# Kernel optimization log

Hardware: AMD Instinct MI355X
Metric: run time of the kernel (lower is better)

Reference implementation:

```python
import jax, jax.numpy as jnp
import numpy as np

N_NODES = 100000
N_EDGES = 3200000
DIM = 128
N_LAYERS = 3
NUM_GRAPHS = 128
BN_EPS = 1e-5
GIN_EPS = 0.0  # eps buffer initialized to 0, train_eps=False


def setup_inputs() -> dict:
    key = jax.random.key(0)
    ks = jax.random.split(key, 12)
    s = 1.0 / np.sqrt(DIM)
    inp = {
        "x": jax.random.normal(ks[0], (N_NODES, DIM), jnp.float32),
        "edge_index": jax.random.randint(ks[1], (2, N_EDGES), 0, N_NODES, jnp.int64),
        "batch": jnp.sort(jax.random.randint(ks[2], (N_NODES,), 0, NUM_GRAPHS, jnp.int64)),
        # node encoder Linear(x_dim, emb_dim)
        "W_node": jax.random.uniform(ks[3], (DIM, DIM), jnp.float32, -s, s),
        "b_node": jax.random.uniform(ks[4], (DIM,), jnp.float32, -s, s),
        # per-layer MLP: Linear -> BatchNorm -> ReLU -> Linear, stacked over layers
        "W1": jax.random.uniform(ks[5], (N_LAYERS, DIM, DIM), jnp.float32, -s, s),
        "b1": jax.random.uniform(ks[6], (N_LAYERS, DIM), jnp.float32, -s, s),
        "gamma": jnp.ones((N_LAYERS, DIM), jnp.float32),
        "beta": jnp.zeros((N_LAYERS, DIM), jnp.float32),
        "W2": jax.random.uniform(ks[7], (N_LAYERS, DIM, DIM), jnp.float32, -s, s),
        "b2": jax.random.uniform(ks[8], (N_LAYERS, DIM), jnp.float32, -s, s),
    }
    return inp


def _batchnorm(y, gamma, beta):
    # training-mode batch statistics over the node dimension (biased variance)
    mean = jnp.mean(y, axis=0)
    var = jnp.mean(jnp.square(y - mean), axis=0)
    return (y - mean) * jax.lax.rsqrt(var + BN_EPS) * gamma + beta


def reference(x, edge_index, batch, W_node, b_node, W1, b1, gamma, beta, W2, b2):
    src, dst = edge_index[0], edge_index[1]
    n = x.shape[0]
    h = x @ W_node + b_node  # [N, D]
    for i in range(N_LAYERS):
        # GINConv: scatter-add gathered neighbor features, eps-residual, MLP
        agg = jax.ops.segment_sum(h[src], dst, num_segments=n)  # [N, D]
        out = agg + (1.0 + GIN_EPS) * h
        y = out @ W1[i] + b1[i]
        y = jax.nn.relu(_batchnorm(y, gamma[i], beta[i]))
        y = y @ W2[i] + b2[i]
        h = jax.nn.relu(y)  # outer ReLU in Encoder.forward (dropout_p=0)
    # global_add_pool
    return jax.ops.segment_sum(h, batch, num_segments=NUM_GRAPHS)  # [G, D]
```

## Files before the change

kernel.cpp:

```cpp
#include <hip/hip_runtime.h>

#define N_NODES 100000
#define M_PAD   100096
#define N_EDGES 3200000
#define DIM 128
#define N_LAYERS 3
#define NUM_GRAPHS 128
#define BN_EPS 1e-5f

#define DST_SHIFT 7
#define BUCKET_NODES 128
#define N_BUCKETS ((N_NODES + BUCKET_NODES - 1) / BUCKET_NODES)
#define BUCKET_CAP 4864
#define EDGES_PER_BLOCK 16384
#define BIN_BLOCKS ((N_EDGES + EDGES_PER_BLOCK - 1) / EDGES_PER_BLOCK)
#define N_BANDS 64

typedef unsigned int uint32;
typedef unsigned short u16;
typedef __attribute__((ext_vector_type(8))) short bf16x8;
typedef __attribute__((ext_vector_type(4))) float f32x4;

__device__ __forceinline__ float bf2f(u16 u) {
    union { uint32 i; float f; } c;
    c.i = ((uint32)u) << 16;
    return c.f;
}
__device__ __forceinline__ u16 f2bf(float f) {
    union { float f; uint32 i; } c;
    c.f = f;
    uint32 i = c.i;
    return (u16)((i + 0x7FFFu + ((i >> 16) & 1u)) >> 16);
}
__device__ __forceinline__ float lo_bf(uint32 v) {
    union { uint32 i; float f; } c;
    c.i = v << 16;
    return c.f;
}
__device__ __forceinline__ float hi_bf(uint32 v) {
    union { uint32 i; float f; } c;
    c.i = v & 0xFFFF0000u;
    return c.f;
}
__device__ __forceinline__ uint32 pack_bf2(float a, float b) {
    return ((uint32)f2bf(b) << 16) | (uint32)f2bf(a);
}
__device__ __forceinline__ void unpack_add8(float* acc, uint4 v) {
    acc[0] += lo_bf(v.x); acc[1] += hi_bf(v.x);
    acc[2] += lo_bf(v.y); acc[3] += hi_bf(v.y);
    acc[4] += lo_bf(v.z); acc[5] += hi_bf(v.z);
    acc[6] += lo_bf(v.w); acc[7] += hi_bf(v.w);
}

__global__ __launch_bounds__(256) void zero_misc(int* __restrict__ gcur,
                                                 float* __restrict__ bn_stats,
                                                 float* __restrict__ outp,
                                                 uint32* __restrict__ aggpad32) {
    int i = blockIdx.x * 256 + threadIdx.x;
    if (i < N_BUCKETS) gcur[i] = 0;
    if (i < N_LAYERS * 2 * DIM) bn_stats[i] = 0.f;
    if (i < NUM_GRAPHS * DIM) outp[i] = 0.f;
    if (i < (M_PAD - N_NODES) * DIM / 2) aggpad32[i] = 0;
}

__global__ __launch_bounds__(256) void bin_by_dst(const int* __restrict__ src,
                                                  const int* __restrict__ dst,
                                                  int* __restrict__ gcur,
                                                  uint32* __restrict__ packed) {
    __shared__ int cnt[N_BUCKETS];
    __shared__ int cur[N_BUCKETS];
    int t = threadIdx.x;
    int e0 = blockIdx.x * EDGES_PER_BLOCK;
    for (int i = t; i < N_BUCKETS; i += 256) cnt[i] = 0;
    __syncthreads();

    for (int j = 0; j < EDGES_PER_BLOCK / 256; ++j) {
        int e = e0 + j * 256 + t;
        if (e < N_EDGES) atomicAdd(&cnt[dst[e] >> DST_SHIFT], 1);
    }
    __syncthreads();
    for (int i = t; i < N_BUCKETS; i += 256) {
        int c = cnt[i];
        cur[i] = c ? atomicAdd(&gcur[i], c) : 0;
    }
    __syncthreads();
    for (int j = 0; j < EDGES_PER_BLOCK / 256; ++j) {
        int e = e0 + j * 256 + t;
        if (e < N_EDGES) {
            int d = dst[e];
            int b = d >> DST_SHIFT;
            int pos = atomicAdd(&cur[b], 1);
            if (pos < BUCKET_CAP)
                packed[(size_t)b * BUCKET_CAP + pos] =
                    (uint32)src[e] | ((uint32)(d & (BUCKET_NODES - 1)) << 17);
        }
    }
}

__global__ void scan_buckets(const int* __restrict__ gcur, int* __restrict__ obase,
                             int* __restrict__ row_ptr) {
    __shared__ int s[N_BUCKETS];
    int t = threadIdx.x;
    for (int i = t; i < N_BUCKETS; i += 256) {
        int c = gcur[i];
        s[i] = (c > BUCKET_CAP) ? BUCKET_CAP : c;
    }
    __syncthreads();
    if (t == 0) {
        int run = 0;
        for (int i = 0; i < N_BUCKETS; ++i) {
            int c = s[i];
            s[i] = run;
            run += c;
        }
        row_ptr[N_NODES] = run;
    }
    __syncthreads();
    for (int i = t; i < N_BUCKETS; i += 256) obase[i] = s[i];
}

__global__ __launch_bounds__(256) void build_buckets(const uint32* __restrict__ packed,
                                                     const int* __restrict__ gcur,
                                                     const int* __restrict__ obase_arr,
                                                     int* __restrict__ row_ptr,
                                                     int* __restrict__ col_src) {
    __shared__ uint32 ed[BUCKET_CAP];
    __shared__ uint32 ed2[BUCKET_CAP];
    __shared__ int bandcur[N_BANDS];
    __shared__ int ncnt[BUCKET_NODES];
    __shared__ int ncur[BUCKET_NODES];
    int b = blockIdx.x, t = threadIdx.x;
    int cnt = gcur[b];
    if (cnt > BUCKET_CAP) cnt = BUCKET_CAP;
    int obase = obase_arr[b];
    int n0 = b * BUCKET_NODES;

    if (t < N_BANDS) bandcur[t] = 0;
    if (t < BUCKET_NODES) ncnt[t] = 0;
    __syncthreads();

    const uint32* reg = packed + (size_t)b * BUCKET_CAP;
    for (int i = t; i < cnt; i += 256) {
        uint32 v = reg[i];
        ed[i] = v;
        atomicAdd(&bandcur[(v & 0x1FFFFu) >> 11], 1);
        atomicAdd(&ncnt[v >> 17], 1);
    }
    __syncthreads();

    if (t == 0) {
        int run = 0;
        for (int w = 0; w < N_BANDS; ++w) {
            int c = bandcur[w];
            bandcur[w] = run;
            run += c;
        }
    }
    int myc = (t < BUCKET_NODES) ? ncnt[t] : 0;
    if (t < BUCKET_NODES) ncur[t] = myc;
    __syncthreads();
    for (int off = 1; off < BUCKET_NODES; off <<= 1) {
        int v = 0;
        if (t < BUCKET_NODES && t >= off) v = ncur[t - off];
        __syncthreads();
        if (t < BUCKET_NODES) ncur[t] += v;
        __syncthreads();
    }
    if (t < BUCKET_NODES) {
        int excl = ncur[t] - myc;
        ncur[t] = excl;
        int gn = n0 + t;
        if (gn < N_NODES) row_ptr[gn] = obase + excl;
    }
    __syncthreads();

    for (int i = t; i < cnt; i += 256) {
        uint32 v = ed[i];
        int p = atomicAdd(&bandcur[(v & 0x1FFFFu) >> 11], 1);
        ed2[p] = v;
    }
    __syncthreads();

    for (int i = t; i < cnt; i += 256) {
        uint32 v = ed2[i];
        int slot = atomicAdd(&ncur[v >> 17], 1);
        col_src[obase + slot] = (int)(v & 0x1FFFFu);
    }
}

__global__ void cvt_wt_all(const float* __restrict__ Wn, const float* __restrict__ W1,
                           const float* __restrict__ W2, u16* __restrict__ WT) {
    int m = blockIdx.x >> 7, n = blockIdx.x & 127, k = threadIdx.x;
    const float* src = (m == 0) ? Wn
                     : (m <= 3) ? W1 + (size_t)(m - 1) * DIM * DIM
                                : W2 + (size_t)(m - 4) * DIM * DIM;
    int L = n * 256 + k * 2;
    int Ls = L ^ ((n & 7) << 4);
    *(u16*)((char*)WT + (size_t)m * 32768 + Ls) = f2bf(src[(size_t)k * DIM + n]);
}

__global__ __launch_bounds__(256) void aggregate_bf(const u16* __restrict__ h,
                                                    const int* __restrict__ row_ptr,
                                                    const int* __restrict__ col_src,
                                                    u16* __restrict__ agg) {
    int wv = (blockIdx.x * 256 + threadIdx.x) >> 6;
    int lane = threadIdx.x & 63;
    int q = lane >> 4, c = lane & 15;
    if (wv >= N_NODES) return;
    int beg = row_ptr[wv], end = row_ptr[wv + 1];
    const uint4* h4 = (const uint4*)h;

    float acc[8];
#pragma unroll
    for (int j = 0; j < 8; ++j) acc[j] = 0.f;

    if (q == 0) {
        uint4 v = h4[(size_t)wv * 16 + c];
        unpack_add8(acc, v);
    }
    int e = beg + q;
    for (; e + 12 < end; e += 16) {
        int i0 = col_src[e];
        int i1 = col_src[e + 4];
        int i2 = col_src[e + 8];
        int i3 = col_src[e + 12];
        uint4 v0 = h4[(size_t)i0 * 16 + c];
        uint4 v1 = h4[(size_t)i1 * 16 + c];
        uint4 v2 = h4[(size_t)i2 * 16 + c];
        uint4 v3 = h4[(size_t)i3 * 16 + c];
        unpack_add8(acc, v0);
        unpack_add8(acc, v1);
        unpack_add8(acc, v2);
        unpack_add8(acc, v3);
    }
    for (; e < end; e += 4) {
        uint4 v0 = h4[(size_t)col_src[e] * 16 + c];
        unpack_add8(acc, v0);
    }
#pragma unroll
    for (int j = 0; j < 8; ++j) {
        acc[j] += __shfl_xor(acc[j], 16);
        acc[j] += __shfl_xor(acc[j], 32);
    }
    if (q == 0) {
        uint4 o;
        o.x = pack_bf2(acc[0], acc[1]);
        o.y = pack_bf2(acc[2], acc[3]);
        o.z = pack_bf2(acc[4], acc[5]);
        o.w = pack_bf2(acc[6], acc[7]);
        *(uint4*)&agg[(size_t)wv * DIM + c * 8] = o;
    }
}

template <int MODE>
__global__ __launch_bounds__(256) void gemm_v2(const void* __restrict__ Av,
                                               const u16* __restrict__ WTs,
                                               const float* __restrict__ bias,
                                               u16* __restrict__ outp,
                                               float* __restrict__ bn_sum,
                                               float* __restrict__ bn_sumsq,
                                               const float* __restrict__ gamma,
                                               const float* __restrict__ beta) {
    __shared__ u16 sB[DIM * DIM];
    __shared__ float sc_[DIM];
    __shared__ float sh_[DIM];
    __shared__ float ls[4][DIM];
    __shared__ float lq[4][DIM];

    int t = threadIdx.x;
    {
        const uint4* Wg = (const uint4*)WTs;
        uint4* sB4 = (uint4*)sB;
#pragma unroll
        for (int i = 0; i < 8; ++i) sB4[i * 256 + t] = Wg[i * 256 + t];
    }
    if (MODE == 2 && t < DIM) {
        const float invN = 1.0f / (float)N_NODES;
        float mean = bn_sum[t] * invN;
        float var = fmaxf(bn_sumsq[t] * invN - mean * mean, 0.f);
        float rs = rsqrtf(var + BN_EPS);
        float sc = gamma[t] * rs;
        sc_[t] = sc;
        sh_[t] = beta[t] - mean * sc;
    }
    __syncthreads();

    int wid = t >> 6, lane = t & 63;
    int hw = lane >> 4, c = lane & 15;
    int row0 = blockIdx.x * 128 + wid * 32;

    bf16x8 a[2][4];
#pragma unroll
    for (int rf = 0; rf < 2; ++rf) {
        int row = row0 + rf * 16 + c;
#pragma unroll
        for (int ks = 0; ks < 4; ++ks) {
            int k0 = ks * 32 + hw * 8;
            if (MODE == 0) {
                const float* xf = (const float*)Av;
                float4 v0 = make_float4(0.f, 0.f, 0.f, 0.f), v1 = v0;
                if (row < N_NODES) {
                    v0 = *(const float4*)&xf[(size_t)row * DIM + k0];
                    v1 = *(const float4*)&xf[(size_t)row * DIM + k0 + 4];
                }
                union { bf16x8 v; u16 u[8]; } ua;
                ua.u[0] = f2bf(v0.x); ua.u[1] = f2bf(v0.y);
                ua.u[2] = f2bf(v0.z); ua.u[3] = f2bf(v0.w);
                ua.u[4] = f2bf(v1.x); ua.u[5] = f2bf(v1.y);
                ua.u[6] = f2bf(v1.z); ua.u[7] = f2bf(v1.w);
                a[rf][ks] = ua.v;
            } else {
                const u16* Ab = (const u16*)Av;
                bf16x8 av = *(const bf16x8*)&Ab[(size_t)row * DIM + k0];
                if (MODE == 2) {
                    union { bf16x8 v; u16 u[8]; } ua;
                    ua.v = av;
#pragma unroll
                    for (int j = 0; j < 8; ++j) {
                        float f = bf2f(ua.u[j]);
                        f = fmaxf(fmaf(f, sc_[k0 + j], sh_[k0 + j]), 0.f);
                        ua.u[j] = f2bf(f);
                    }
                    av = ua.v;
                }
                a[rf][ks] = av;
            }
        }
    }

    f32x4 acc[2][8];
#pragma unroll
    for (int rf = 0; rf < 2; ++rf)
#pragma unroll
        for (int nf = 0; nf < 8; ++nf) acc[rf][nf] = (f32x4){0.f, 0.f, 0.f, 0.f};

    int swz = (c & 7) << 4;
#pragma unroll
    for (int ks = 0; ks < 4; ++ks) {
#pragma unroll
        for (int nf = 0; nf < 8; ++nf) {
            int L = (nf * 4096 + c * 256 + ks * 64 + hw * 16) ^ swz;
            bf16x8 b = *(const bf16x8*)((const char*)sB + L);
            acc[0][nf] = __builtin_amdgcn_mfma_f32_16x16x32_bf16(a[0][ks], b, acc[0][nf], 0, 0, 0);
            acc[1][nf] = __builtin_amdgcn_mfma_f32_16x16x32_bf16(a[1][ks], b, acc[1][nf], 0, 0, 0);
        }
    }

    float s_[8], q_[8];
#pragma unroll
    for (int nf = 0; nf < 8; ++nf) { s_[nf] = 0.f; q_[nf] = 0.f; }

#pragma unroll
    for (int rf = 0; rf < 2; ++rf) {
        int rbase = row0 + rf * 16 + hw * 4;
#pragma unroll
        for (int nf = 0; nf < 8; ++nf) {
            float bv = bias[nf * 16 + c];
#pragma unroll
            for (int r = 0; r < 4; ++r) {
                float v = acc[rf][nf][r] + bv;
                if (MODE == 2) v = fmaxf(v, 0.f);
                outp[(size_t)(rbase + r) * DIM + nf * 16 + c] = f2bf(v);
                if (MODE == 1) {
                    float m = (rbase + r < N_NODES) ? v : 0.f;
                    s_[nf] += m;
                    q_[nf] += m * m;
                }
            }
        }
    }

    if (MODE == 1) {
#pragma unroll
        for (int nf = 0; nf < 8; ++nf) {
            s_[nf] += __shfl_xor(s_[nf], 16);
            s_[nf] += __shfl_xor(s_[nf], 32);
            q_[nf] += __shfl_xor(q_[nf], 16);
            q_[nf] += __shfl_xor(q_[nf], 32);
        }
        if (lane < 16) {
#pragma unroll
            for (int nf = 0; nf < 8; ++nf) {
                ls[wid][nf * 16 + c] = s_[nf];
                lq[wid][nf * 16 + c] = q_[nf];
            }
        }
        __syncthreads();
        if (t < DIM) {
            atomicAdd(&bn_sum[t], ls[0][t] + ls[1][t] + ls[2][t] + ls[3][t]);
            atomicAdd(&bn_sumsq[t], lq[0][t] + lq[1][t] + lq[2][t] + lq[3][t]);
        }
    }
}

__global__ __launch_bounds__(256) void pool_bf(const u16* __restrict__ h,
                                               const int* __restrict__ batch,
                                               float* __restrict__ out) {
    int wv = (blockIdx.x * 256 + threadIdx.x) >> 6;
    int lane = threadIdx.x & 63;
    int base = wv * 32;
    if (base >= N_NODES) return;
    int end = base + 32;
    if (end > N_NODES) end = N_NODES;
    const uint32* h32 = (const uint32*)h;
    float ax = 0.f, ay = 0.f;
    int curg = batch[base];
    for (int n = base; n < end; ++n) {
        int g = batch[n];
        if (g != curg) {
            atomicAdd(&out[curg * DIM + lane * 2], ax);
            atomicAdd(&out[curg * DIM + lane * 2 + 1], ay);
            ax = 0.f;
            ay = 0.f;
            curg = g;
        }
        uint32 v = h32[(size_t)n * 64 + lane];
        ax += lo_bf(v);
        ay += hi_bf(v);
    }
    atomicAdd(&out[curg * DIM + lane * 2], ax);
    atomicAdd(&out[curg * DIM + lane * 2 + 1], ay);
}

extern "C" void kernel_launch(void* const* d_in, const int* in_sizes, int n_in,
                              void* d_out, int out_size, void* d_ws, size_t ws_size,
                              hipStream_t stream) {
    const float* x     = (const float*)d_in[0];
    const int*   ei    = (const int*)d_in[1];
    const int*   batch = (const int*)d_in[2];
    const float* Wn    = (const float*)d_in[3];
    const float* bnode = (const float*)d_in[4];
    const float* W1    = (const float*)d_in[5];
    const float* b1    = (const float*)d_in[6];
    const float* gamma = (const float*)d_in[7];
    const float* beta  = (const float*)d_in[8];
    const float* W2    = (const float*)d_in[9];
    const float* b2    = (const float*)d_in[10];
    float* out = (float*)d_out;

    const int* e_src = ei;
    const int* e_dst = ei + N_EDGES;

    const size_t MD = (size_t)M_PAD * DIM;
    u16* h   = (u16*)d_ws;
    u16* agg = h + MD;
    u16* y   = agg + MD;
    u16* WT  = y + MD;
    int* row_ptr = (int*)(WT + 7 * DIM * DIM);
    int* col_src = row_ptr + N_NODES + 1;
    int* gcur    = col_src + N_EDGES;
    int* obase   = gcur + N_BUCKETS;
    float* bn_stats = (float*)(obase + N_BUCKETS);
    uint32* packed = (uint32*)y;

    const int GEMM_BLOCKS = M_PAD / 128;
    const int AGG_BLOCKS = (N_NODES * 64 + 255) / 256;
    const int POOL_BLOCKS = (((N_NODES + 31) / 32) * 64 + 255) / 256;

    zero_misc<<<64, 256, 0, stream>>>(gcur, bn_stats, out,
                                      (uint32*)(agg + (size_t)N_NODES * DIM));
    bin_by_dst<<<BIN_BLOCKS, 256, 0, stream>>>(e_src, e_dst, gcur, packed);
    scan_buckets<<<1, 256, 0, stream>>>(gcur, obase, row_ptr);
    build_buckets<<<N_BUCKETS, 256, 0, stream>>>(packed, gcur, obase, row_ptr, col_src);

    cvt_wt_all<<<7 * DIM, DIM, 0, stream>>>(Wn, W1, W2, WT);

    gemm_v2<0><<<GEMM_BLOCKS, 256, 0, stream>>>(x, WT, bnode, h, nullptr,
                                                nullptr, nullptr, nullptr);

    for (int i = 0; i < N_LAYERS; ++i) {
        float* bn_sum = bn_stats + (size_t)i * 2 * DIM;
        float* bn_sumsq = bn_sum + DIM;
        aggregate_bf<<<AGG_BLOCKS, 256, 0, stream>>>(h, row_ptr, col_src, agg);
        gemm_v2<1><<<GEMM_BLOCKS, 256, 0, stream>>>(
            agg, WT + (size_t)(1 + i) * DIM * DIM, b1 + i * DIM, y, bn_sum,
            bn_sumsq, nullptr, nullptr);
        gemm_v2<2><<<GEMM_BLOCKS, 256, 0, stream>>>(
            y, WT + (size_t)(4 + i) * DIM * DIM, b2 + i * DIM, h, bn_sum,
            bn_sumsq, gamma + i * DIM, beta + i * DIM);
    }

    pool_bf<<<POOL_BLOCKS, 256, 0, stream>>>(h, batch, out);
}
```

Before: 615.0 us.

## Aggregate two nodes per 16-lane group and prefetch GEMM A-tiles before weight staging

```diff
diff --git a/kernel.cpp b/kernel.cpp
--- a/kernel.cpp
+++ b/kernel.cpp
@@ -203,53 +203,66 @@
                                                     const int* __restrict__ row_ptr,
                                                     const int* __restrict__ col_src,
                                                     u16* __restrict__ agg) {
-    int wv = (blockIdx.x * 256 + threadIdx.x) >> 6;
-    int lane = threadIdx.x & 63;
-    int q = lane >> 4, c = lane & 15;
-    if (wv >= N_NODES) return;
-    int beg = row_ptr[wv], end = row_ptr[wv + 1];
+    int t = threadIdx.x;
+    int quad = (blockIdx.x * 256 + t) >> 4;
+    int c = t & 15;
+    int nA = quad * 2;
+    if (nA >= N_NODES) return;
+    int nB = nA + 1;
     const uint4* h4 = (const uint4*)h;
 
-    float acc[8];
-#pragma unroll
-    for (int j = 0; j < 8; ++j) acc[j] = 0.f;
-
-    if (q == 0) {
-        uint4 v = h4[(size_t)wv * 16 + c];
-        unpack_add8(acc, v);
-    }
-    int e = beg + q;
-    for (; e + 12 < end; e += 16) {
-        int i0 = col_src[e];
-        int i1 = col_src[e + 4];
-        int i2 = col_src[e + 8];
-        int i3 = col_src[e + 12];
-        uint4 v0 = h4[(size_t)i0 * 16 + c];
-        uint4 v1 = h4[(size_t)i1 * 16 + c];
-        uint4 v2 = h4[(size_t)i2 * 16 + c];
-        uint4 v3 = h4[(size_t)i3 * 16 + c];
-        unpack_add8(acc, v0);
-        unpack_add8(acc, v1);
-        unpack_add8(acc, v2);
-        unpack_add8(acc, v3);
-    }
-    for (; e < end; e += 4) {
-        uint4 v0 = h4[(size_t)col_src[e] * 16 + c];
-        unpack_add8(acc, v0);
-    }
-#pragma unroll
-    for (int j = 0; j < 8; ++j) {
-        acc[j] += __shfl_xor(acc[j], 16);
-        acc[j] += __shfl_xor(acc[j], 32);
-    }
-    if (q == 0) {
-        uint4 o;
-        o.x = pack_bf2(acc[0], acc[1]);
-        o.y = pack_bf2(acc[2], acc[3]);
-        o.z = pack_bf2(acc[4], acc[5]);
-        o.w = pack_bf2(acc[6], acc[7]);
-        *(uint4*)&agg[(size_t)wv * DIM + c * 8] = o;
-    }
+    int begA = row_ptr[nA], endA = row_ptr[nA + 1];
+    int begB = row_ptr[nB], endB = row_ptr[nB + 1];
+    int lenA = endA - begA, lenB = endB - begB;
+    int m = lenA < lenB ? lenA : lenB;
+
+    float a_[8], b_[8];
+#pragma unroll
+    for (int j = 0; j < 8; ++j) { a_[j] = 0.f; b_[j] = 0.f; }
+
+    {
+        uint4 sA = h4[(size_t)nA * 16 + c];
+        uint4 sB = h4[(size_t)nB * 16 + c];
+        unpack_add8(a_, sA);
+        unpack_add8(b_, sB);
+    }
+
+    int i = 0;
+    for (; i + 2 <= m; i += 2) {
+        int iA0 = col_src[begA + i], iA1 = col_src[begA + i + 1];
+        int iB0 = col_src[begB + i], iB1 = col_src[begB + i + 1];
+        uint4 vA0 = h4[(size_t)iA0 * 16 + c];
+        uint4 vB0 = h4[(size_t)iB0 * 16 + c];
+        uint4 vA1 = h4[(size_t)iA1 * 16 + c];
+        uint4 vB1 = h4[(size_t)iB1 * 16 + c];
+        unpack_add8(a_, vA0);
+        unpack_add8(b_, vB0);
+        unpack_add8(a_, vA1);
+        unpack_add8(b_, vB1);
+    }
+    if (i < m) {
+        uint4 vA = h4[(size_t)col_src[begA + i] * 16 + c];
+        uint4 vB = h4[(size_t)col_src[begB + i] * 16 + c];
+        unpack_add8(a_, vA);
+        unpack_add8(b_, vB);
+        ++i;
+    }
+    for (int e = begA + i; e < endA; ++e) {
+        uint4 v = h4[(size_t)col_src[e] * 16 + c];
+        unpack_add8(a_, v);
+    }
+    for (int e = begB + i; e < endB; ++e) {
+        uint4 v = h4[(size_t)col_src[e] * 16 + c];
+        unpack_add8(b_, v);
+    }
+
+    uint4 oA, oB;
+    oA.x = pack_bf2(a_[0], a_[1]); oA.y = pack_bf2(a_[2], a_[3]);
+    oA.z = pack_bf2(a_[4], a_[5]); oA.w = pack_bf2(a_[6], a_[7]);
+    oB.x = pack_bf2(b_[0], b_[1]); oB.y = pack_bf2(b_[2], b_[3]);
+    oB.z = pack_bf2(b_[4], b_[5]); oB.w = pack_bf2(b_[6], b_[7]);
+    *(uint4*)&agg[(size_t)nA * DIM + c * 8] = oA;
+    *(uint4*)&agg[(size_t)nB * DIM + c * 8] = oB;
 }
 
 template <int MODE>
@@ -268,6 +281,33 @@
     __shared__ float lq[4][DIM];
 
     int t = threadIdx.x;
+    int wid = t >> 6, lane = t & 63;
+    int hw = lane >> 4, c = lane & 15;
+    int row0 = blockIdx.x * 128 + wid * 32;
+
+    bf16x8 a[2][4];
+    float4 af[2][4][2];
+#pragma unroll
+    for (int rf = 0; rf < 2; ++rf) {
+        int row = row0 + rf * 16 + c;
+#pragma unroll
+        for (int ks = 0; ks < 4; ++ks) {
+            int k0 = ks * 32 + hw * 8;
+            if (MODE == 0) {
+                const float* xf = (const float*)Av;
+                af[rf][ks][0] = make_float4(0.f, 0.f, 0.f, 0.f);
+                af[rf][ks][1] = af[rf][ks][0];
+                if (row < N_NODES) {
+                    af[rf][ks][0] = *(const float4*)&xf[(size_t)row * DIM + k0];
+                    af[rf][ks][1] = *(const float4*)&xf[(size_t)row * DIM + k0 + 4];
+                }
+            } else {
+                const u16* Ab = (const u16*)Av;
+                a[rf][ks] = *(const bf16x8*)&Ab[(size_t)row * DIM + k0];
+            }
+        }
+    }
+
     {
         const uint4* Wg = (const uint4*)WTs;
         uint4* sB4 = (uint4*)sB;
@@ -285,45 +325,29 @@
     }
     __syncthreads();
 
-    int wid = t >> 6, lane = t & 63;
-    int hw = lane >> 4, c = lane & 15;
-    int row0 = blockIdx.x * 128 + wid * 32;
-
-    bf16x8 a[2][4];
 #pragma unroll
     for (int rf = 0; rf < 2; ++rf) {
-        int row = row0 + rf * 16 + c;
 #pragma unroll
         for (int ks = 0; ks < 4; ++ks) {
             int k0 = ks * 32 + hw * 8;
             if (MODE == 0) {
-                const float* xf = (const float*)Av;
-                float4 v0 = make_float4(0.f, 0.f, 0.f, 0.f), v1 = v0;
-                if (row < N_NODES) {
-                    v0 = *(const float4*)&xf[(size_t)row * DIM + k0];
-                    v1 = *(const float4*)&xf[(size_t)row * DIM + k0 + 4];
-                }
                 union { bf16x8 v; u16 u[8]; } ua;
+                float4 v0 = af[rf][ks][0], v1 = af[rf][ks][1];
                 ua.u[0] = f2bf(v0.x); ua.u[1] = f2bf(v0.y);
                 ua.u[2] = f2bf(v0.z); ua.u[3] = f2bf(v0.w);
                 ua.u[4] = f2bf(v1.x); ua.u[5] = f2bf(v1.y);
                 ua.u[6] = f2bf(v1.z); ua.u[7] = f2bf(v1.w);
                 a[rf][ks] = ua.v;
-            } else {
-                const u16* Ab = (const u16*)Av;
-                bf16x8 av = *(const bf16x8*)&Ab[(size_t)row * DIM + k0];
-                if (MODE == 2) {
-                    union { bf16x8 v; u16 u[8]; } ua;
-                    ua.v = av;
-#pragma unroll
-                    for (int j = 0; j < 8; ++j) {
-                        float f = bf2f(ua.u[j]);
-                        f = fmaxf(fmaf(f, sc_[k0 + j], sh_[k0 + j]), 0.f);
-                        ua.u[j] = f2bf(f);
-                    }
-                    av = ua.v;
+            } else if (MODE == 2) {
+                union { bf16x8 v; u16 u[8]; } ua;
+                ua.v = a[rf][ks];
+#pragma unroll
+                for (int j = 0; j < 8; ++j) {
+                    float f = bf2f(ua.u[j]);
+                    f = fmaxf(fmaf(f, sc_[k0 + j], sh_[k0 + j]), 0.f);
+                    ua.u[j] = f2bf(f);
                 }
-                a[rf][ks] = av;
+                a[rf][ks] = ua.v;
             }
         }
     }
@@ -454,7 +478,7 @@
     uint32* packed = (uint32*)y;
 
     const int GEMM_BLOCKS = M_PAD / 128;
-    const int AGG_BLOCKS = (N_NODES * 64 + 255) / 256;
+    const int AGG_BLOCKS = (N_NODES / 2 * 16 + 255) / 256;
     const int POOL_BLOCKS = (((N_NODES + 31) / 32) * 64 + 255) / 256;
 
     zero_misc<<<64, 256, 0, stream>>>(gcur, bn_stats, out,
```

New measurement: 653.2 us. 6.2% more time.

## Remap aggregate block order across XCDs and prefetch GEMM A-tiles before weight load

Applied to the files above, without the earlier changes.

```diff
diff --git a/kernel.cpp b/kernel.cpp
--- a/kernel.cpp
+++ b/kernel.cpp
@@ -15,6 +15,9 @@
 #define EDGES_PER_BLOCK 16384
 #define BIN_BLOCKS ((N_EDGES + EDGES_PER_BLOCK - 1) / EDGES_PER_BLOCK)
 #define N_BANDS 64
+
+#define AGG_BLOCKS 25000
+#define AGG_CHUNK  (AGG_BLOCKS / 8)
 
 typedef unsigned int uint32;
 typedef unsigned short u16;
@@ -203,7 +206,8 @@
                                                     const int* __restrict__ row_ptr,
                                                     const int* __restrict__ col_src,
                                                     u16* __restrict__ agg) {
-    int wv = (blockIdx.x * 256 + threadIdx.x) >> 6;
+    int wg = (blockIdx.x & 7) * AGG_CHUNK + (blockIdx.x >> 3);
+    int wv = wg * 4 + (threadIdx.x >> 6);
     int lane = threadIdx.x & 63;
     int q = lane >> 4, c = lane & 15;
     if (wv >= N_NODES) return;
@@ -268,6 +272,33 @@
     __shared__ float lq[4][DIM];
 
     int t = threadIdx.x;
+    int wid = t >> 6, lane = t & 63;
+    int hw = lane >> 4, c = lane & 15;
+    int row0 = blockIdx.x * 128 + wid * 32;
+
+    bf16x8 a[2][4];
+    float4 af[2][4][2];
+#pragma unroll
+    for (int rf = 0; rf < 2; ++rf) {
+        int row = row0 + rf * 16 + c;
+#pragma unroll
+        for (int ks = 0; ks < 4; ++ks) {
+            int k0 = ks * 32 + hw * 8;
+            if (MODE == 0) {
+                const float* xf = (const float*)Av;
+                af[rf][ks][0] = make_float4(0.f, 0.f, 0.f, 0.f);
+                af[rf][ks][1] = af[rf][ks][0];
+                if (row < N_NODES) {
+                    af[rf][ks][0] = *(const float4*)&xf[(size_t)row * DIM + k0];
+                    af[rf][ks][1] = *(const float4*)&xf[(size_t)row * DIM + k0 + 4];
+                }
+            } else {
+                const u16* Ab = (const u16*)Av;
+                a[rf][ks] = *(const bf16x8*)&Ab[(size_t)row * DIM + k0];
+            }
+        }
+    }
+
     {
         const uint4* Wg = (const uint4*)WTs;
         uint4* sB4 = (uint4*)sB;
@@ -285,45 +316,29 @@
     }
     __syncthreads();
 
-    int wid = t >> 6, lane = t & 63;
-    int hw = lane >> 4, c = lane & 15;
-    int row0 = blockIdx.x * 128 + wid * 32;
-
-    bf16x8 a[2][4];
 #pragma unroll
     for (int rf = 0; rf < 2; ++rf) {
-        int row = row0 + rf * 16 + c;
 #pragma unroll
         for (int ks = 0; ks < 4; ++ks) {
             int k0 = ks * 32 + hw * 8;
             if (MODE == 0) {
-                const float* xf = (const float*)Av;
-                float4 v0 = make_float4(0.f, 0.f, 0.f, 0.f), v1 = v0;
-                if (row < N_NODES) {
-                    v0 = *(const float4*)&xf[(size_t)row * DIM + k0];
-                    v1 = *(const float4*)&xf[(size_t)row * DIM + k0 + 4];
-                }
                 union { bf16x8 v; u16 u[8]; } ua;
+                float4 v0 = af[rf][ks][0], v1 = af[rf][ks][1];
                 ua.u[0] = f2bf(v0.x); ua.u[1] = f2bf(v0.y);
                 ua.u[2] = f2bf(v0.z); ua.u[3] = f2bf(v0.w);
                 ua.u[4] = f2bf(v1.x); ua.u[5] = f2bf(v1.y);
                 ua.u[6] = f2bf(v1.z); ua.u[7] = f2bf(v1.w);
                 a[rf][ks] = ua.v;
-            } else {
-                const u16* Ab = (const u16*)Av;
-                bf16x8 av = *(const bf16x8*)&Ab[(size_t)row * DIM + k0];
-                if (MODE == 2) {
-                    union { bf16x8 v; u16 u[8]; } ua;
-                    ua.v = av;
-#pragma unroll
-                    for (int j = 0; j < 8; ++j) {
-                        float f = bf2f(ua.u[j]);
-                        f = fmaxf(fmaf(f, sc_[k0 + j], sh_[k0 + j]), 0.f);
-                        ua.u[j] = f2bf(f);
-                    }
-                    av = ua.v;
+            } else if (MODE == 2) {
+                union { bf16x8 v; u16 u[8]; } ua;
+                ua.v = a[rf][ks];
+#pragma unroll
+                for (int j = 0; j < 8; ++j) {
+                    float f = bf2f(ua.u[j]);
+                    f = fmaxf(fmaf(f, sc_[k0 + j], sh_[k0 + j]), 0.f);
+                    ua.u[j] = f2bf(f);
                 }
-                a[rf][ks] = av;
+                a[rf][ks] = ua.v;
             }
         }
     }
@@ -454,7 +469,6 @@
     uint32* packed = (uint32*)y;
 
     const int GEMM_BLOCKS = M_PAD / 128;
-    const int AGG_BLOCKS = (N_NODES * 64 + 255) / 256;
     const int POOL_BLOCKS = (((N_NODES + 31) / 32) * 64 + 255) / 256;
 
     zero_misc<<<64, 256, 0, stream>>>(gcur, bn_stats, out,
```

Measured after the change: 611.2 us. No clear change (-0.6%).
